# Performance work log

Measured on AMD Instinct MI355X. Metric: run time of the kernel, lower is better.

The kernel has to match this reference:

```python
import jax, jax.numpy as jnp
import numpy as np
from jax import lax

B, KLEN, QLEN = 16, 1500, 200
KDIM = QDIM = ADIM = ODIM = 512
H_MA, H_CA, W = 4, 2, 4
H_TOT = H_MA * H_CA
EPS = 1e-6
NEG_INF = -1e9


def _excl_cumsum(x):
    # [a,b,c] -> [0,a,a+b] along last axis
    c = jnp.cumsum(x, axis=-1)
    return jnp.concatenate([jnp.zeros_like(c[..., :1]), c[..., :-1]], axis=-1)


def _moving_sum(x, back, forward):
    # sum over window [j-back, j+forward] along last axis
    k = x.shape[-1]
    pad = [(0, 0)] * (x.ndim - 1) + [(back, forward)]
    c = jnp.cumsum(jnp.pad(x, pad), axis=-1)
    c = jnp.concatenate([jnp.zeros_like(c[..., :1]), c], axis=-1)
    return c[..., back + forward + 1:] - c[..., :k]


def setup_inputs() -> dict:
    key = jax.random.key(0)
    ks = jax.random.split(key, 16)
    sK = KDIM ** -0.5
    sA = ADIM ** -0.5
    inp = {
        'key':   jax.random.normal(ks[0], (B, KLEN, KDIM), jnp.float32),
        'value': jax.random.normal(ks[1], (B, KLEN, KDIM), jnp.float32),
        'query': jax.random.normal(ks[2], (B, QLEN, QDIM), jnp.float32),
        'mask':  jnp.ones((B, QLEN, KLEN), jnp.bool_),
        # monotonic energy params
        'Wk_ma': jax.random.normal(ks[3], (KDIM, ADIM), jnp.float32) * sK,
        'bk_ma': jnp.zeros((ADIM,), jnp.float32),
        'Wq_ma': jax.random.normal(ks[4], (QDIM, ADIM), jnp.float32) * sK,
        'bq_ma': jnp.zeros((ADIM,), jnp.float32),
        'r':     jnp.array(-4.0, jnp.float32),
        # chunk energy params
        'Wk_ca': jax.random.normal(ks[5], (KDIM, ADIM), jnp.float32) * sK,
        'bk_ca': jnp.zeros((ADIM,), jnp.float32),
        'Wq_ca': jax.random.normal(ks[6], (QDIM, ADIM), jnp.float32) * sK,
        'bq_ca': jnp.zeros((ADIM,), jnp.float32),
        # value / output projections
        'Wv':    jax.random.normal(ks[7], (KDIM, ADIM), jnp.float32) * sK,
        'bv':    jnp.zeros((ADIM,), jnp.float32),
        'Wout':  jax.random.normal(ks[8], (ADIM, ODIM), jnp.float32) * sA,
        'bout':  jnp.zeros((ODIM,), jnp.float32),
    }
    return inp


def _mocha_forward(key, value, query, mask,
                   Wk_ma, bk_ma, Wq_ma, bq_ma, r,
                   Wk_ca, bk_ca, Wq_ca, bq_ca,
                   Wv, bv, Wout, bout):
    bs = key.shape[0]
    d_ma = ADIM // H_MA
    d_ca = ADIM // H_TOT
    maskb = mask[:, None]  # [B,1,q,k]

    # ---- monotonic energy: [B,H_ma,q,k] ----
    k_ma = (key @ Wk_ma + bk_ma).reshape(bs, KLEN, H_MA, d_ma)
    q_ma = (query @ Wq_ma + bq_ma).reshape(bs, QLEN, H_MA, d_ma)
    e_ma = jnp.einsum('bqhd,bkhd->bhqk', q_ma, k_ma) / jnp.sqrt(jnp.float32(d_ma)) + r
    e_ma = jnp.where(maskb, e_ma, NEG_INF)

    # ---- parallel monotonic attention (cumprod/cumsum recurrence) ----
    p_choose = jax.nn.sigmoid(e_ma)  # [B,H_ma,q,k]
    # safe exclusive cumprod of (1 - p) in log space
    cumprod_1mp = jnp.exp(_excl_cumsum(jnp.log(jnp.clip(1.0 - p_choose, EPS, 1.0))))

    aw0 = jnp.zeros((bs, H_MA, KLEN), p_choose.dtype).at[:, :, 0].set(1.0)
    p_t = jnp.moveaxis(p_choose, 2, 0)      # [q,B,H_ma,k]
    cp_t = jnp.moveaxis(cumprod_1mp, 2, 0)  # [q,B,H_ma,k]

    def step(aw_prev, inp):
        p_i, cp_i = inp
        denom = jnp.clip(cp_i, EPS, 1.0)
        aw = p_i * cp_i * jnp.cumsum(aw_prev / denom, axis=-1)
        return aw, aw

    _, alpha = lax.scan(step, aw0, (p_t, cp_t))
    alpha = jnp.moveaxis(alpha, 0, 2)  # [B,H_ma,q,k]

    # ---- chunk energy: [B,H_ma*H_ca,q,k] ----
    k_ca = (key @ Wk_ca + bk_ca).reshape(bs, KLEN, H_TOT, d_ca)
    q_ca = (query @ Wq_ca + bq_ca).reshape(bs, QLEN, H_TOT, d_ca)
    e_ca = jnp.einsum('bqhd,bkhd->bhqk', q_ca, k_ca) / jnp.sqrt(jnp.float32(d_ca))
    e_ca = jnp.where(maskb, e_ca, NEG_INF)

    # ---- efficient chunkwise attention (windowed softmax, window W) ----
    u = e_ca.reshape(bs, H_MA, H_CA, QLEN, KLEN)
    u = u - jnp.max(u, axis=-1, keepdims=True)
    softmax_exp = jnp.maximum(jnp.exp(u), 1e-5)
    denoms = _moving_sum(softmax_exp, back=W - 1, forward=0)
    beta = softmax_exp * _moving_sum(alpha[:, :, None] / denoms, back=0, forward=W - 1)
    beta = beta.reshape(bs, H_TOT, QLEN, KLEN)

    # ---- multihead value aggregation + output projection ----
    v = (value @ Wv + bv).reshape(bs, KLEN, H_TOT, d_ca)
    cv = jnp.einsum('bhqk,bkhd->bqhd', beta, v).reshape(bs, QLEN, ADIM)
    return cv @ Wout + bout  # [B,q,odim]


def reference(key, value, query, mask,
              Wk_ma, bk_ma, Wq_ma, bq_ma, r,
              Wk_ca, bk_ca, Wq_ca, bq_ca,
              Wv, bv, Wout, bout):
    return _mocha_forward(key, value, query, mask,
                          Wk_ma, bk_ma, Wq_ma, bq_ma, r,
                          Wk_ca, bk_ca, Wq_ca, bq_ca,
                          Wv, bv, Wout, bout)
```

## Files before the change

### kernel.cpp

```cpp
#include <hip/hip_runtime.h>
#include <hip/hip_bf16.h>
#include <type_traits>

constexpr int BS    = 16;
constexpr int KLEN  = 1500;
constexpr int QLEN  = 200;
constexpr int DIM   = 512;
constexpr int H_MA  = 4;
constexpr int H_CA  = 2;
constexpr int H_TOT = 8;
constexpr int D_MA  = 128;
constexpr int D_CA  = 64;
constexpr float EPS = 1e-6f;
constexpr float SC_MA = 0.08838834764831845f;
constexpr float SC_CA = 0.125f;


template<int ACT, bool TRANSB>
__global__ __launch_bounds__(256)
void gemm_kernel(const float* __restrict__ A, const float* __restrict__ Bm,
                 const float* __restrict__ bias, const float* __restrict__ addc_ptr,
                 float* __restrict__ C, int M, int N, int K,
                 int lda, int ldb, int ldc, int H,
                 long long sAb, long long sAh, long long sBb, long long sBh,
                 long long sCb, long long sCh, float scale)
{
    __shared__ float As[16][64];
    __shared__ float Bsh[16][64];
    int z = blockIdx.z;
    int bb = z / H, hh = z - bb * H;
    A  += (long long)bb * sAb + (long long)hh * sAh;
    Bm += (long long)bb * sBb + (long long)hh * sBh;
    C  += (long long)bb * sCb + (long long)hh * sCh;

    int m0 = blockIdx.y * 64, n0 = blockIdx.x * 64;
    int tid = threadIdx.x;
    int tx = tid & 15, ty = tid >> 4;
    int r4 = tid >> 2, c4 = (tid & 3) * 4;

    float acc[4][4] = {};

    for (int k0 = 0; k0 < K; k0 += 16) {
        {
            int gr = m0 + r4;
            #pragma unroll
            for (int j = 0; j < 4; j++) {
                int gc = k0 + c4 + j;
                As[c4 + j][r4] = (gr < M && gc < K) ? A[(long long)gr * lda + gc] : 0.f;
            }
        }
        if (!TRANSB) {
            int kk = tid >> 4, nn = (tid & 15) * 4;
            int gk = k0 + kk;
            #pragma unroll
            for (int j = 0; j < 4; j++) {
                int gn = n0 + nn + j;
                Bsh[kk][nn + j] = (gk < K && gn < N) ? Bm[(long long)gk * ldb + gn] : 0.f;
            }
        } else {
            int gn = n0 + r4;
            #pragma unroll
            for (int j = 0; j < 4; j++) {
                int gk = k0 + c4 + j;
                Bsh[c4 + j][r4] = (gn < N && gk < K) ? Bm[(long long)gn * ldb + gk] : 0.f;
            }
        }
        __syncthreads();

        #pragma unroll
        for (int kk = 0; kk < 16; kk++) {
            float a[4], b[4];
            #pragma unroll
            for (int i = 0; i < 4; i++) a[i] = As[kk][ty * 4 + i];
            #pragma unroll
            for (int j = 0; j < 4; j++) b[j] = Bsh[kk][tx * 4 + j];
            #pragma unroll
            for (int i = 0; i < 4; i++)
                #pragma unroll
                for (int j = 0; j < 4; j++)
                    acc[i][j] += a[i] * b[j];
        }
        __syncthreads();
    }

    float addc = addc_ptr ? addc_ptr[0] : 0.f;
    #pragma unroll
    for (int i = 0; i < 4; i++) {
        int gm = m0 + ty * 4 + i;
        if (gm >= M) continue;
        #pragma unroll
        for (int j = 0; j < 4; j++) {
            int gn = n0 + tx * 4 + j;
            if (gn >= N) continue;
            float v = acc[i][j] * scale + addc;
            if (bias) v += bias[gn];
            if (ACT == 1) v = 1.f / (1.f + expf(-v));
            C[(long long)gm * ldc + gn] = v;
        }
    }
}

__global__ __launch_bounds__(256)
void gemm128p_kernel(const float* __restrict__ A, const float* __restrict__ B,
                     const float* __restrict__ bias, float* __restrict__ C,
                     int M, int N, int K, int lda, int ldb, int ldc)
{
    __shared__ float As[16][132];
    __shared__ float Bs[16][132];

    int m0 = blockIdx.y * 128, n0 = blockIdx.x * 128;
    int tid = threadIdx.x;
    int tx = tid & 15, ty = tid >> 4;
    int lr = tid >> 2;
    int lc = (tid & 3) * 4;
    int bkr = tid >> 4;
    int bn  = (tid & 15) * 8;
    int bnp = bn + (bn >> 5);
    int bcp = tx * 8 + ((tx * 8) >> 5);

    float acc[8][8] = {};

    for (int k0 = 0; k0 < K; k0 += 16) {
        #pragma unroll
        for (int i = 0; i < 2; i++) {
            int gr = m0 + lr + i * 64;
            float4 av = make_float4(0.f, 0.f, 0.f, 0.f);
            if (gr < M)
                av = *reinterpret_cast<const float4*>(&A[(long long)gr * lda + k0 + lc]);
            As[lc + 0][lr + i * 64] = av.x;
            As[lc + 1][lr + i * 64] = av.y;
            As[lc + 2][lr + i * 64] = av.z;
            As[lc + 3][lr + i * 64] = av.w;
        }
        {
            float4 b0 = make_float4(0.f,0.f,0.f,0.f), b1 = b0;
            if (n0 + bn + 7 < N) {
                const float* brow = &B[(long long)(k0 + bkr) * ldb + n0 + bn];
                b0 = *reinterpret_cast<const float4*>(brow);
                b1 = *reinterpret_cast<const float4*>(brow + 4);
            } else {
                float tmp[8];
                #pragma unroll
                for (int j = 0; j < 8; j++)
                    tmp[j] = (n0 + bn + j < N) ? B[(long long)(k0 + bkr) * ldb + n0 + bn + j] : 0.f;
                b0 = make_float4(tmp[0],tmp[1],tmp[2],tmp[3]);
                b1 = make_float4(tmp[4],tmp[5],tmp[6],tmp[7]);
            }
            *reinterpret_cast<float4*>(&Bs[bkr][bnp])     = b0;
            *reinterpret_cast<float4*>(&Bs[bkr][bnp + 4]) = b1;
        }
        __syncthreads();

        #pragma unroll
        for (int kk = 0; kk < 16; kk++) {
            float4 a0 = *reinterpret_cast<const float4*>(&As[kk][ty * 8]);
            float4 a1 = *reinterpret_cast<const float4*>(&As[kk][ty * 8 + 4]);
            float4 c0 = *reinterpret_cast<const float4*>(&Bs[kk][bcp]);
            float4 c1 = *reinterpret_cast<const float4*>(&Bs[kk][bcp + 4]);
            float a[8] = {a0.x,a0.y,a0.z,a0.w,a1.x,a1.y,a1.z,a1.w};
            float b[8] = {c0.x,c0.y,c0.z,c0.w,c1.x,c1.y,c1.z,c1.w};
            #pragma unroll
            for (int i = 0; i < 8; i++)
                #pragma unroll
                for (int j = 0; j < 8; j++)
                    acc[i][j] += a[i] * b[j];
        }
        __syncthreads();
    }

    #pragma unroll
    for (int i = 0; i < 8; i++) {
        int gm = m0 + ty * 8 + i;
        if (gm >= M) continue;
        #pragma unroll
        for (int j = 0; j < 8; j++) {
            int gn = n0 + tx * 8 + j;
            if (gn < N)
                C[(long long)gm * ldc + gn] = acc[i][j] + (bias ? bias[gn] : 0.f);
        }
    }
}

__device__ __forceinline__ void gemm128_body(
    const float* __restrict__ A, const float* __restrict__ B,
    const float* __restrict__ bias, float* __restrict__ C,
    int M, int N, int K, int lda, int ldb, int ldc,
    int m0, int n0, float (*As)[128], float (*Bs)[128])
{
    int tid = threadIdx.x;
    int tx = tid & 15, ty = tid >> 4;
    int lr = tid >> 2;
    int lc = (tid & 3) * 4;
    int bkr = tid >> 4;
    int bn  = (tid & 15) * 8;

    float acc[8][8] = {};

    for (int k0 = 0; k0 < K; k0 += 16) {
        #pragma unroll
        for (int i = 0; i < 2; i++) {
            int gr = m0 + lr + i * 64;
            float4 av = make_float4(0.f, 0.f, 0.f, 0.f);
            if (gr < M)
                av = *reinterpret_cast<const float4*>(&A[(long long)gr * lda + k0 + lc]);
            As[lc + 0][lr + i * 64] = av.x;
            As[lc + 1][lr + i * 64] = av.y;
            As[lc + 2][lr + i * 64] = av.z;
            As[lc + 3][lr + i * 64] = av.w;
        }
        {
            float4 b0 = make_float4(0.f,0.f,0.f,0.f), b1 = b0;
            if (n0 + bn + 7 < N) {
                const float* brow = &B[(long long)(k0 + bkr) * ldb + n0 + bn];
                b0 = *reinterpret_cast<const float4*>(brow);
                b1 = *reinterpret_cast<const float4*>(brow + 4);
            } else {
                float tmp[8];
                #pragma unroll
                for (int j = 0; j < 8; j++)
                    tmp[j] = (n0 + bn + j < N) ? B[(long long)(k0 + bkr) * ldb + n0 + bn + j] : 0.f;
                b0 = make_float4(tmp[0],tmp[1],tmp[2],tmp[3]);
                b1 = make_float4(tmp[4],tmp[5],tmp[6],tmp[7]);
            }
            *reinterpret_cast<float4*>(&Bs[bkr][bn])     = b0;
            *reinterpret_cast<float4*>(&Bs[bkr][bn + 4]) = b1;
        }
        __syncthreads();

        #pragma unroll
        for (int kk = 0; kk < 16; kk++) {
            float4 a0 = *reinterpret_cast<const float4*>(&As[kk][ty * 8]);
            float4 a1 = *reinterpret_cast<const float4*>(&As[kk][ty * 8 + 4]);
            float4 c0 = *reinterpret_cast<const float4*>(&Bs[kk][tx * 8]);
            float4 c1 = *reinterpret_cast<const float4*>(&Bs[kk][tx * 8 + 4]);
            float a[8] = {a0.x,a0.y,a0.z,a0.w,a1.x,a1.y,a1.z,a1.w};
            float b[8] = {c0.x,c0.y,c0.z,c0.w,c1.x,c1.y,c1.z,c1.w};
            #pragma unroll
            for (int i = 0; i < 8; i++)
                #pragma unroll
                for (int j = 0; j < 8; j++)
                    acc[i][j] += a[i] * b[j];
        }
        __syncthreads();
    }

    #pragma unroll
    for (int i = 0; i < 8; i++) {
        int gm = m0 + ty * 8 + i;
        if (gm >= M) continue;
        #pragma unroll
        for (int j = 0; j < 8; j++) {
            int gn = n0 + tx * 8 + j;
            if (gn < N)
                C[(long long)gm * ldc + gn] = acc[i][j] + (bias ? bias[gn] : 0.f);
        }
    }
}

__device__ inline float block_excl_scan(float tot, float* lds4)
{
    int lane = threadIdx.x & 63, wv = threadIdx.x >> 6;
    float incl = tot;
    #pragma unroll
    for (int d = 1; d < 64; d <<= 1) {
        float n = __shfl_up(incl, d, 64);
        if (lane >= d) incl += n;
    }
    if (lane == 63) lds4[wv] = incl;
    __syncthreads();
    float base = 0.f;
    #pragma unroll
    for (int w = 0; w < 3; w++)
        if (w < wv) base += lds4[w];
    float r = base + incl - tot;
    __syncthreads();
    return r;
}

__device__ void alpha_body(const float* __restrict__ P, float* __restrict__ AL,
                           int bh, float* lds4)
{
    int tid = threadIdx.x, k0 = tid * 6;
    bool act = (tid < 250);
    long long base = (long long)bh * QLEN * KLEN;
    const float* Pb = P + base;
    float* Ab = AL + base;

    float awp[6];
    #pragma unroll
    for (int j = 0; j < 6; j++) awp[j] = ((k0 + j) == 0) ? 1.f : 0.f;

    float pj[6];
    if (act) {
        const float2* p2 = reinterpret_cast<const float2*>(Pb + k0);
        float2 a = p2[0], b = p2[1], c = p2[2];
        pj[0] = a.x; pj[1] = a.y; pj[2] = b.x; pj[3] = b.y; pj[4] = c.x; pj[5] = c.y;
    } else {
        #pragma unroll
        for (int j = 0; j < 6; j++) pj[j] = 0.f;
    }

    for (int q = 0; q < QLEN; q++) {
        float pjn[6] = {0.f,0.f,0.f,0.f,0.f,0.f};
        if (act && q + 1 < QLEN) {
            const float2* p2n = reinterpret_cast<const float2*>(Pb + (long long)(q + 1) * KLEN + k0);
            float2 a = p2n[0], b = p2n[1], c = p2n[2];
            pjn[0] = a.x; pjn[1] = a.y; pjn[2] = b.x; pjn[3] = b.y; pjn[4] = c.x; pjn[5] = c.y;
        }

        float lpre[6], lrun = 0.f;
        #pragma unroll
        for (int j = 0; j < 6; j++) {
            lpre[j] = lrun;
            float v = fminf(fmaxf(1.f - pj[j], EPS), 1.f);
            lrun += act ? logf(v) : 0.f;
        }
        float lbase = block_excl_scan(lrun, lds4);
        float cj[6];
        #pragma unroll
        for (int j = 0; j < 6; j++) cj[j] = expf(lbase + lpre[j]);
        float pre[6], run = 0.f;
        #pragma unroll
        for (int j = 0; j < 6; j++) {
            float dn = fminf(fmaxf(cj[j], EPS), 1.f);
            run += act ? (awp[j] / dn) : 0.f;
            pre[j] = run;
        }
        float sbase = block_excl_scan(run, lds4);
        #pragma unroll
        for (int j = 0; j < 6; j++)
            awp[j] = pj[j] * cj[j] * (sbase + pre[j]);
        if (act) {
            float* arow = Ab + (long long)q * KLEN + k0;
            #pragma unroll
            for (int j = 0; j < 6; j++) arow[j] = awp[j];
        }
        #pragma unroll
        for (int j = 0; j < 6; j++) pj[j] = pjn[j];
    }
}

__global__ __launch_bounds__(256)
void alpha_kernel(const float* __restrict__ P, float* __restrict__ AL)
{
    __shared__ float lds4[4];
    alpha_body(P, AL, blockIdx.x, lds4);
}

__global__ __launch_bounds__(256)
void packed_kernel(const float* __restrict__ P, float* __restrict__ AL,
                   const float* __restrict__ key, const float* __restrict__ Wk,
                   const float* __restrict__ bk, float* __restrict__ kout,
                   const float* __restrict__ query, const float* __restrict__ Wq,
                   const float* __restrict__ bq, float* __restrict__ qout)
{
    __shared__ float As[16][128];
    __shared__ float Bs[16][128];
    int bid = blockIdx.x;
    if (bid < 64) { alpha_body(P, AL, bid, &As[0][0]); return; }
    bid -= 64;
    if (bid < 752) {
        int n0 = (bid & 3) * 128, m0 = (bid >> 2) * 128;
        gemm128_body(key, Wk, bk, kout, BS*KLEN, DIM, DIM, DIM, DIM, DIM, m0, n0, As, Bs);
        return;
    }
    bid -= 752;
    int n0 = (bid & 3) * 128, m0 = (bid >> 2) * 128;
    gemm128_body(query, Wq, bq, qout, BS*QLEN, DIM, DIM, DIM, DIM, DIM, m0, n0, As, Bs);
}

__device__ __forceinline__ void score_tile(
    const float* __restrict__ Qb, const float* __restrict__ Kb,
    int q0, int kbase, float (*As)[68], float (*Bsh)[68], float acc[4][4])
{
    int tid = threadIdx.x;
    int tx = tid & 15, ty = tid >> 4;
    int m = tid >> 2, c4 = (tid & 3) * 4;
    for (int d0 = 0; d0 < 64; d0 += 16) {
        int gq = q0 + m;
        int gk = kbase + m;
        #pragma unroll
        for (int j = 0; j < 4; j++) {
            As[c4 + j][m]  = (gq < QLEN) ? Qb[(long long)gq * DIM + d0 + c4 + j] : 0.f;
            Bsh[c4 + j][m] = (gk < KLEN) ? Kb[(long long)gk * DIM + d0 + c4 + j] : 0.f;
        }
        __syncthreads();
        #pragma unroll
        for (int dd = 0; dd < 16; dd++) {
            float a[4], b[4];
            #pragma unroll
            for (int i = 0; i < 4; i++) a[i] = As[dd][ty * 4 + i];
            #pragma unroll
            for (int j = 0; j < 4; j++) b[j] = Bsh[dd][tx * 4 + j];
            #pragma unroll
            for (int i = 0; i < 4; i++)
                #pragma unroll
                for (int j = 0; j < 4; j++)
                    acc[i][j] += a[i] * b[j];
        }
        __syncthreads();
    }
}

__global__ __launch_bounds__(256)
void fbpv_kernel(const float* __restrict__ qca, const float* __restrict__ kca,
                 const float* __restrict__ vpr, const float* __restrict__ alp,
                 float* __restrict__ CV)
{
    __shared__ float Ss[64][65];
    __shared__ float Tt[64][65];
    __shared__ float Bbt[64][68];
    __shared__ float Vs[64][68];
    __shared__ float As[16][68];
    __shared__ float Bsh[16][68];
    __shared__ float Cse[64][3];
    __shared__ float Ctt[64][3];

    int qt = blockIdx.x;
    int z  = blockIdx.y;
    int h = z % H_TOT, b = z / H_TOT, hma = h >> 1;
    int q0 = qt * 64;

    const float* Qb = qca + (long long)b * QLEN * DIM + h * D_CA;
    const float* Kb = kca + (long long)b * KLEN * DIM + h * D_CA;
    const float* Vb = vpr + (long long)b * KLEN * DIM + h * D_CA;
    const float* Ab = alp + (long long)(b * H_MA + hma) * QLEN * KLEN;

    int tid = threadIdx.x;
    int tx = tid & 15, ty = tid >> 4;

    if (tid < 192) { int r = tid & 63, c = tid >> 6; Cse[r][c] = 0.f; Ctt[r][c] = 0.f; }
    __syncthreads();

    float pv[4][4] = {};
    for (int kt = 0; kt < 24; ++kt) {
        int kbase = kt * 64;

        float alv[16];
        {
            int r = tid >> 2, jb = (tid & 3) * 16;
            int q = q0 + r;
            if (q < QLEN) {
                #pragma unroll
                for (int u = 0; u < 16; u += 4) {
                    int g = kbase + jb + u;
                    if (g + 3 < KLEN) {
                        float4 t = *reinterpret_cast<const float4*>(&Ab[(long long)q * KLEN + g]);
                        alv[u] = t.x; alv[u+1] = t.y; alv[u+2] = t.z; alv[u+3] = t.w;
                    } else {
                        #pragma unroll
                        for (int v = 0; v < 4; v++)
                            alv[u+v] = (g + v < KLEN) ? Ab[(long long)q * KLEN + g + v] : 0.f;
                    }
                }
            } else {
                #pragma unroll
                for (int u = 0; u < 16; u++) alv[u] = 0.f;
            }
        }

        float acc[4][4] = {};
        score_tile(Qb, Kb, q0, kbase, As, Bsh, acc);

        #pragma unroll
        for (int i = 0; i < 4; i++) {
            int r = ty * 4 + i;
            #pragma unroll
            for (int jr = 0; jr < 4; jr++) {
                int j = (jr + ty) & 3;
                int g = kbase + tx * 4 + j;
                float se = (g < KLEN) ? fmaxf(expf(acc[i][j] * SC_CA), 1e-5f) : 0.f;
                Ss[r][tx * 4 + j] = se;
            }
        }
        __syncthreads();

        {
            int r = tid >> 2, jb = (tid & 3) * 16;
            int q = q0 + r;
            #pragma unroll
            for (int u = 0; u < 16; u++) {
                int j = jb + u;
                int g = kbase + j;
                float s0 = (j >= 3) ? Ss[r][j-3] : Cse[r][j];
                float s1 = (j >= 2) ? Ss[r][j-2] : Cse[r][j+1];
                float s2 = (j >= 1) ? Ss[r][j-1] : Cse[r][j+2];
                float s3 = Ss[r][j];
                float denom = s0 + s1 + s2 + s3;
                Tt[r][j] = (g < KLEN && q < QLEN) ? alv[u] / denom : 0.f;
            }
        }
        __syncthreads();

        {
            int r = tid >> 2, jb = (tid & 3) * 16;
            #pragma unroll
            for (int u = 0; u < 16; u++) {
                int j = jb + u;
                float sex = (j < 3) ? Cse[r][j] : Ss[r][j-3];
                float t0  = (j < 3) ? Ctt[r][j] : Tt[r][j-3];
                float t1  = (j < 2) ? Ctt[r][j+1] : Tt[r][j-2];
                float t2  = (j < 1) ? Ctt[r][j+2] : Tt[r][j-1];
                float t3  = Tt[r][j];
                Bbt[j][r] = sex * (t0 + t1 + t2 + t3);
            }
            int jv = tid >> 2, d0 = (tid & 3) * 16;
            int g = kbase - 3 + jv;
            if (g >= 0 && g < KLEN) {
                #pragma unroll
                for (int u = 0; u < 16; u += 4) {
                    float4 t = *reinterpret_cast<const float4*>(&Vb[(long long)g * DIM + d0 + u]);
                    *reinterpret_cast<float4*>(&Vs[jv][d0 + u]) = t;
                }
            } else {
                #pragma unroll
                for (int u = 0; u < 16; u += 4)
                    *reinterpret_cast<float4*>(&Vs[jv][d0 + u]) = make_float4(0.f,0.f,0.f,0.f);
            }
        }
        __syncthreads();

        if (tid < 64) {
            int r = tid;
            Cse[r][0] = Ss[r][61]; Cse[r][1] = Ss[r][62]; Cse[r][2] = Ss[r][63];
            Ctt[r][0] = Tt[r][61]; Ctt[r][1] = Tt[r][62]; Ctt[r][2] = Tt[r][63];
        }

        #pragma unroll 4
        for (int jj = 0; jj < 64; ++jj) {
            float4 a4 = *reinterpret_cast<const float4*>(&Bbt[jj][ty * 4]);
            float4 b4 = *reinterpret_cast<const float4*>(&Vs[jj][tx * 4]);
            float a[4] = {a4.x, a4.y, a4.z, a4.w};
            float bv[4] = {b4.x, b4.y, b4.z, b4.w};
            #pragma unroll
            for (int i = 0; i < 4; i++)
                #pragma unroll
                for (int j = 0; j < 4; j++)
                    pv[i][j] += a[i] * bv[j];
        }
        __syncthreads();
    }

    #pragma unroll
    for (int i = 0; i < 4; i++) {
        int q = q0 + ty * 4 + i;
        if (q >= QLEN) continue;
        #pragma unroll
        for (int j = 0; j < 4; j++)
            CV[((long long)b * QLEN + q) * DIM + h * D_CA + tx * 4 + j] = pv[i][j];
    }
}

extern "C" void kernel_launch(void* const* d_in, const int* in_sizes, int n_in,
                              void* d_out, int out_size, void* d_ws, size_t ws_size,
                              hipStream_t stream)
{
    if (n_in < 17) return;
    const int expect[17] = {
        BS*KLEN*DIM, BS*KLEN*DIM, BS*QLEN*DIM, BS*QLEN*KLEN,
        DIM*DIM, DIM, DIM*DIM, DIM, 1,
        DIM*DIM, DIM, DIM*DIM, DIM, DIM*DIM, DIM, DIM*DIM, DIM
    };
    for (int i = 0; i < 17; i++)
        if (in_sizes[i] != expect[i]) return;
    if (out_size != BS*QLEN*DIM) return;

    const float* key   = (const float*)d_in[0];
    const float* value = (const float*)d_in[1];
    const float* query = (const float*)d_in[2];
    const float* Wk_ma = (const float*)d_in[4];
    const float* bk_ma = (const float*)d_in[5];
    const float* Wq_ma = (const float*)d_in[6];
    const float* bq_ma = (const float*)d_in[7];
    const float* rptr  = (const float*)d_in[8];
    const float* Wk_ca = (const float*)d_in[9];
    const float* bk_ca = (const float*)d_in[10];
    const float* Wq_ca = (const float*)d_in[11];
    const float* bq_ca = (const float*)d_in[12];
    const float* Wv    = (const float*)d_in[13];
    const float* bv    = (const float*)d_in[14];
    const float* Wout  = (const float*)d_in[15];
    const float* bout  = (const float*)d_in[16];
    float* out = (float*)d_out;

    const size_t SZ_KPROJ = (size_t)BS * KLEN * DIM;
    const size_t SZ_QPROJ = (size_t)BS * QLEN * DIM;
    const size_t SZ_SCORE = (size_t)BS * H_MA * QLEN * KLEN;

    float* ws = (float*)d_ws;
    size_t wsf = ws_size / sizeof(float);
    dim3 blk(256);

    const size_t MAIN_FLOATS = 2*SZ_SCORE + SZ_KPROJ + 2*SZ_QPROJ;
    if (wsf >= MAIN_FLOATS) {
        float* alp  = ws;
        float* k_ma = ws;
        float* q_ma = ws + SZ_KPROJ;
        float* Pb   = ws + SZ_SCORE;
        float* vpr  = Pb;
        float* k_ca = ws + 2*SZ_SCORE;
        float* q_ca = k_ca + SZ_KPROJ;
        float* cv   = q_ca + SZ_QPROJ;

        gemm128p_kernel<<<dim3(4,188), blk, 0, stream>>>(key, Wk_ma, bk_ma, k_ma,
            BS*KLEN, DIM, DIM, DIM, DIM, DIM);
        gemm128p_kernel<<<dim3(4,25), blk, 0, stream>>>(query, Wq_ma, bq_ma, q_ma,
            BS*QLEN, DIM, DIM, DIM, DIM, DIM);

        gemm_kernel<1,true><<<dim3(24,4,BS*H_MA), blk, 0, stream>>>(
            q_ma, k_ma, nullptr, rptr, Pb, QLEN, KLEN, D_MA, DIM, DIM, KLEN,
            H_MA,
            (long long)QLEN*DIM, (long long)D_MA,
            (long long)KLEN*DIM, (long long)D_MA,
            (long long)H_MA*QLEN*KLEN, (long long)QLEN*KLEN,
            SC_MA);

        packed_kernel<<<dim3(916), blk, 0, stream>>>(
            Pb, alp, key, Wk_ca, bk_ca, k_ca, query, Wq_ca, bq_ca, q_ca);

        gemm128p_kernel<<<dim3(4,188), blk, 0, stream>>>(value, Wv, bv, vpr,
            BS*KLEN, DIM, DIM, DIM, DIM, DIM);

        fbpv_kernel<<<dim3(4, BS*H_TOT), blk, 0, stream>>>(q_ca, k_ca, vpr, alp, cv);

        gemm128p_kernel<<<dim3(4,25), blk, 0, stream>>>(cv, Wout, bout, out,
            BS*QLEN, DIM, DIM, DIM, DIM, DIM);
        return;
    }

    float* alp  = ws;
    float* k_ma = ws;
    float* q_ma = ws + SZ_KPROJ;
    float* Pb   = ws + SZ_SCORE;
    float* k_ca = ws + SZ_SCORE;
    float* q_ca = k_ca + SZ_KPROJ;
    float* vpr  = q_ca + SZ_QPROJ;
    float* cv   = vpr + SZ_KPROJ;
    const size_t BASE_FLOATS = SZ_SCORE + SZ_KPROJ + SZ_QPROJ + SZ_KPROJ + SZ_QPROJ;
    if (ws_size < BASE_FLOATS * sizeof(float)) return;

    gemm128p_kernel<<<dim3(4,188), blk, 0, stream>>>(key, Wk_ma, bk_ma, k_ma,
        BS*KLEN, DIM, DIM, DIM, DIM, DIM);
    gemm128p_kernel<<<dim3(4,25), blk, 0, stream>>>(query, Wq_ma, bq_ma, q_ma,
        BS*QLEN, DIM, DIM, DIM, DIM, DIM);

    gemm_kernel<1,true><<<dim3(24,4,BS*H_MA), blk, 0, stream>>>(
        q_ma, k_ma, nullptr, rptr, Pb, QLEN, KLEN, D_MA, DIM, DIM, KLEN,
        H_MA,
        (long long)QLEN*DIM, (long long)D_MA,
        (long long)KLEN*DIM, (long long)D_MA,
        (long long)H_MA*QLEN*KLEN, (long long)QLEN*KLEN,
        SC_MA);

    alpha_kernel<<<dim3(BS*H_MA), blk, 0, stream>>>(Pb, alp);

    gemm128p_kernel<<<dim3(4,188), blk, 0, stream>>>(key, Wk_ca, bk_ca, k_ca,
        BS*KLEN, DIM, DIM, DIM, DIM, DIM);
    gemm128p_kernel<<<dim3(4,25), blk, 0, stream>>>(query, Wq_ca, bq_ca, q_ca,
        BS*QLEN, DIM, DIM, DIM, DIM, DIM);
    gemm128p_kernel<<<dim3(4,188), blk, 0, stream>>>(value, Wv, bv, vpr,
        BS*KLEN, DIM, DIM, DIM, DIM, DIM);

    fbpv_kernel<<<dim3(4, BS*H_TOT), blk, 0, stream>>>(q_ca, k_ca, vpr, alp, cv);

    gemm128p_kernel<<<dim3(4,25), blk, 0, stream>>>(cv, Wout, bout, out,
        BS*QLEN, DIM, DIM, DIM, DIM, DIM);
}
```

Measured before the change: 1.649 ms.

## Run alpha recurrence in one wavefront with product scan and no block barriers

Rewrites the monotonic-attention alpha recurrence so a single 64-lane wavefront handles a whole row, 24 elements per lane. The cumulative product of (1-p) now comes from a multiplicative shuffle scan instead of a log/exp sum scan, removing the LDS block scans and their barriers. Loads and stores use float4, and reciprocals use rcp intrinsics in alpha and fbpv. The score tile reads LDS as float4. Risks: more register pressure, slightly different precision from product and rcp versus log/exp and division, and only 64 blocks of 64 threads for a serial 200-step loop.

```diff
diff --git a/kernel.cpp b/kernel.cpp
--- a/kernel.cpp
+++ b/kernel.cpp
@@ -257,94 +257,108 @@
     }
 }
 
-__device__ inline float block_excl_scan(float tot, float* lds4)
-{
-    int lane = threadIdx.x & 63, wv = threadIdx.x >> 6;
-    float incl = tot;
-    #pragma unroll
-    for (int d = 1; d < 64; d <<= 1) {
-        float n = __shfl_up(incl, d, 64);
-        if (lane >= d) incl += n;
-    }
-    if (lane == 63) lds4[wv] = incl;
-    __syncthreads();
-    float base = 0.f;
-    #pragma unroll
-    for (int w = 0; w < 3; w++)
-        if (w < wv) base += lds4[w];
-    float r = base + incl - tot;
-    __syncthreads();
-    return r;
-}
-
-__device__ void alpha_body(const float* __restrict__ P, float* __restrict__ AL,
-                           int bh, float* lds4)
-{
-    int tid = threadIdx.x, k0 = tid * 6;
-    bool act = (tid < 250);
+__device__ void alpha_body_w64(const float* __restrict__ P, float* __restrict__ AL, int bh)
+{
+    int lane = threadIdx.x & 63;
+    int k0 = lane * 24;
+    bool full = (k0 + 23 < KLEN);
     long long base = (long long)bh * QLEN * KLEN;
     const float* Pb = P + base;
     float* Ab = AL + base;
 
-    float awp[6];
+    float awp[24];
     #pragma unroll
-    for (int j = 0; j < 6; j++) awp[j] = ((k0 + j) == 0) ? 1.f : 0.f;
-
-    float pj[6];
-    if (act) {
-        const float2* p2 = reinterpret_cast<const float2*>(Pb + k0);
-        float2 a = p2[0], b = p2[1], c = p2[2];
-        pj[0] = a.x; pj[1] = a.y; pj[2] = b.x; pj[3] = b.y; pj[4] = c.x; pj[5] = c.y;
+    for (int j = 0; j < 24; j++) awp[j] = (k0 + j == 0) ? 1.f : 0.f;
+
+    float pj[24];
+    if (full) {
+        #pragma unroll
+        for (int u = 0; u < 24; u += 4) {
+            float4 t = *reinterpret_cast<const float4*>(Pb + k0 + u);
+            pj[u] = t.x; pj[u+1] = t.y; pj[u+2] = t.z; pj[u+3] = t.w;
+        }
     } else {
         #pragma unroll
-        for (int j = 0; j < 6; j++) pj[j] = 0.f;
+        for (int j = 0; j < 24; j++) pj[j] = (k0 + j < KLEN) ? Pb[k0 + j] : 0.f;
     }
 
     for (int q = 0; q < QLEN; q++) {
-        float pjn[6] = {0.f,0.f,0.f,0.f,0.f,0.f};
-        if (act && q + 1 < QLEN) {
-            const float2* p2n = reinterpret_cast<const float2*>(Pb + (long long)(q + 1) * KLEN + k0);
-            float2 a = p2n[0], b = p2n[1], c = p2n[2];
-            pjn[0] = a.x; pjn[1] = a.y; pjn[2] = b.x; pjn[3] = b.y; pjn[4] = c.x; pjn[5] = c.y;
-        }
-
-        float lpre[6], lrun = 0.f;
-        #pragma unroll
-        for (int j = 0; j < 6; j++) {
-            lpre[j] = lrun;
+        float pjn[24];
+        if (q + 1 < QLEN) {
+            const float* pn = Pb + (long long)(q + 1) * KLEN;
+            if (full) {
+                #pragma unroll
+                for (int u = 0; u < 24; u += 4) {
+                    float4 t = *reinterpret_cast<const float4*>(pn + k0 + u);
+                    pjn[u] = t.x; pjn[u+1] = t.y; pjn[u+2] = t.z; pjn[u+3] = t.w;
+                }
+            } else {
+                #pragma unroll
+                for (int j = 0; j < 24; j++) pjn[j] = (k0 + j < KLEN) ? pn[k0 + j] : 0.f;
+            }
+        } else {
+            #pragma unroll
+            for (int j = 0; j < 24; j++) pjn[j] = 0.f;
+        }
+
+        float mpre[24], mrun = 1.f;
+        #pragma unroll
+        for (int j = 0; j < 24; j++) {
+            mpre[j] = mrun;
             float v = fminf(fmaxf(1.f - pj[j], EPS), 1.f);
-            lrun += act ? logf(v) : 0.f;
-        }
-        float lbase = block_excl_scan(lrun, lds4);
-        float cj[6];
-        #pragma unroll
-        for (int j = 0; j < 6; j++) cj[j] = expf(lbase + lpre[j]);
-        float pre[6], run = 0.f;
-        #pragma unroll
-        for (int j = 0; j < 6; j++) {
+            mrun *= v;
+        }
+        float incl = mrun;
+        #pragma unroll
+        for (int d = 1; d < 64; d <<= 1) {
+            float n = __shfl_up(incl, d, 64);
+            if (lane >= d) incl *= n;
+        }
+        float mbase = __shfl_up(incl, 1, 64);
+        if (lane == 0) mbase = 1.f;
+
+        float cj[24], pre[24], run = 0.f;
+        #pragma unroll
+        for (int j = 0; j < 24; j++) {
+            cj[j] = mbase * mpre[j];
             float dn = fminf(fmaxf(cj[j], EPS), 1.f);
-            run += act ? (awp[j] / dn) : 0.f;
+            run += awp[j] * __builtin_amdgcn_rcpf(dn);
             pre[j] = run;
         }
-        float sbase = block_excl_scan(run, lds4);
-        #pragma unroll
-        for (int j = 0; j < 6; j++)
+        float sincl = run;
+        #pragma unroll
+        for (int d = 1; d < 64; d <<= 1) {
+            float n = __shfl_up(sincl, d, 64);
+            if (lane >= d) sincl += n;
+        }
+        float sbase = __shfl_up(sincl, 1, 64);
+        if (lane == 0) sbase = 0.f;
+
+        #pragma unroll
+        for (int j = 0; j < 24; j++)
             awp[j] = pj[j] * cj[j] * (sbase + pre[j]);
-        if (act) {
-            float* arow = Ab + (long long)q * KLEN + k0;
-            #pragma unroll
-            for (int j = 0; j < 6; j++) arow[j] = awp[j];
-        }
-        #pragma unroll
-        for (int j = 0; j < 6; j++) pj[j] = pjn[j];
-    }
-}
-
-__global__ __launch_bounds__(256)
+
+        float* arow = Ab + (long long)q * KLEN + k0;
+        if (full) {
+            #pragma unroll
+            for (int u = 0; u < 24; u += 4) {
+                float4 t = make_float4(awp[u], awp[u+1], awp[u+2], awp[u+3]);
+                *reinterpret_cast<float4*>(arow + u) = t;
+            }
+        } else {
+            #pragma unroll
+            for (int j = 0; j < 24; j++)
+                if (k0 + j < KLEN) arow[j] = awp[j];
+        }
+        #pragma unroll
+        for (int j = 0; j < 24; j++) pj[j] = pjn[j];
+    }
+}
+
+__global__ __launch_bounds__(64)
 void alpha_kernel(const float* __restrict__ P, float* __restrict__ AL)
 {
-    __shared__ float lds4[4];
-    alpha_body(P, AL, blockIdx.x, lds4);
+    alpha_body_w64(P, AL, blockIdx.x);
 }
 
 __global__ __launch_bounds__(256)
@@ -357,7 +371,10 @@
     __shared__ float As[16][128];
     __shared__ float Bs[16][128];
     int bid = blockIdx.x;
-    if (bid < 64) { alpha_body(P, AL, bid, &As[0][0]); return; }
+    if (bid < 64) {
+        if (threadIdx.x < 64) alpha_body_w64(P, AL, bid);
+        return;
+    }
     bid -= 64;
     if (bid < 752) {
         int n0 = (bid & 3) * 128, m0 = (bid >> 2) * 128;
@@ -387,11 +404,10 @@
         __syncthreads();
         #pragma unroll
         for (int dd = 0; dd < 16; dd++) {
-            float a[4], b[4];
-            #pragma unroll
-            for (int i = 0; i < 4; i++) a[i] = As[dd][ty * 4 + i];
-            #pragma unroll
-            for (int j = 0; j < 4; j++) b[j] = Bsh[dd][tx * 4 + j];
+            float4 a4 = *reinterpret_cast<const float4*>(&As[dd][ty * 4]);
+            float4 b4 = *reinterpret_cast<const float4*>(&Bsh[dd][tx * 4]);
+            float a[4] = {a4.x, a4.y, a4.z, a4.w};
+            float b[4] = {b4.x, b4.y, b4.z, b4.w};
             #pragma unroll
             for (int i = 0; i < 4; i++)
                 #pragma unroll
@@ -487,7 +503,7 @@
                 float s2 = (j >= 1) ? Ss[r][j-1] : Cse[r][j+2];
                 float s3 = Ss[r][j];
                 float denom = s0 + s1 + s2 + s3;
-                Tt[r][j] = (g < KLEN && q < QLEN) ? alv[u] / denom : 0.f;
+                Tt[r][j] = (g < KLEN && q < QLEN) ? alv[u] * __builtin_amdgcn_rcpf(denom) : 0.f;
             }
         }
         __syncthreads();
@@ -652,7 +668,7 @@
         (long long)H_MA*QLEN*KLEN, (long long)QLEN*KLEN,
         SC_MA);
 
-    alpha_kernel<<<dim3(BS*H_MA), blk, 0, stream>>>(Pb, alp);
+    alpha_kernel<<<dim3(BS*H_MA), dim3(64), 0, stream>>>(Pb, alp);
 
     gemm128p_kernel<<<dim3(4,188), blk, 0, stream>>>(key, Wk_ca, bk_ca, k_ca,
         BS*KLEN, DIM, DIM, DIM, DIM, DIM);
```

New measurement: 1.660 ms. About the same (+0.6%).
